# Performance work log

Hardware: AMD Instinct MI355X
Metric: run time of the kernel (lower is better)

The kernel has to match this reference:

```python
import jax, jax.numpy as jnp
import numpy as np

CLAMP_LO, CLAMP_HI, CLAMP_GATE_MAX = -10.0, 10.0, 10.0
E, TOPK = 8, 2
M, K, N = 2048, 2048, 1408  # tokens, hidden_dim, intermediate_dim
CAPACITY = 2 * (M * TOPK // E)


def setup_inputs() -> dict:
    key = jax.random.key(0)
    ks = jax.random.split(key, 6)
    bk = 1.0 / np.sqrt(K)  # kaiming_uniform(a=sqrt(5)) bound = 1/sqrt(fan_in)
    bn = 1.0 / np.sqrt(N)
    return {
        "flat_h": jax.random.normal(ks[0], (M, K), jnp.float32),
        "flat_idx": jax.random.randint(ks[1], (M, TOPK), 0, E),
        "flat_gate": jax.random.uniform(ks[2], (M, TOPK), jnp.float32),
        "gate_weight": jax.random.uniform(ks[3], (E, N, K), jnp.float32, -bk, bk),
        "up_weight": jax.random.uniform(ks[4], (E, N, K), jnp.float32, -bk, bk),
        "down_weight": jax.random.uniform(ks[5], (E, K, N), jnp.float32, -bn, bn),
    }


def reference(flat_h, flat_idx, flat_gate, gate_weight, up_weight, down_weight):
    m, top_k = flat_idx.shape
    k = flat_h.shape[1]
    e = gate_weight.shape[0]
    r = m * top_k

    expert_id = flat_idx.reshape(-1)                                   # (R,)
    gate = flat_gate.reshape(-1)                                       # (R,)
    token_index = jnp.repeat(jnp.arange(m, dtype=jnp.int32), top_k)    # (R,)

    # stable sort rows by expert id (mirrors torch.argsort(..., stable=True))
    sort_idx = jnp.argsort(expert_id, stable=True)
    sorted_eid = expert_id[sort_idx]
    tok_sorted = token_index[sort_idx]
    gate_sorted = gate[sort_idx]

    # position of each sorted row inside its expert group
    counts = jnp.bincount(expert_id, length=e)
    starts = jnp.concatenate([jnp.zeros(1, counts.dtype), jnp.cumsum(counts)[:-1]])
    pos = jnp.arange(r) - starts[sorted_eid]                           # (R,)

    # dispatch: scatter sorted tokens into fixed-capacity (E, C, K) buffer
    buf = jnp.zeros((e, CAPACITY, k), flat_h.dtype)
    buf = buf.at[sorted_eid, pos].set(flat_h[tok_sorted])

    # grouped GEMMs: weights stored (E, out, in) like nn.Linear
    g = jnp.einsum("eck,enk->ecn", buf, gate_weight)
    g = jnp.minimum(g, CLAMP_GATE_MAX)
    u = jnp.clip(jnp.einsum("eck,enk->ecn", buf, up_weight), CLAMP_LO, CLAMP_HI)
    h = jax.nn.silu(g) * u                                             # SwiGLU (E, C, N)
    d = jnp.einsum("ecn,ekn->eck", h, down_weight)                     # (E, C, K)

    # combine: gather each routed row back, weight by gate, sum over top_k slots
    expert_out = d[sorted_eid, pos]                                    # (R, K)
    weighted = expert_out * gate_sorted[:, None]
    out = jnp.zeros((m, k), flat_h.dtype).at[tok_sorted].add(weighted)
    return out
```

## Files before the change

### kernel.cpp

```cpp
#include <hip/hip_runtime.h>
#include <hip/hip_bf16.h>

#define M_TOK 2048
#define KDIM 2048
#define NDIM 1408
#define NEXP 8
#define RROWS (M_TOK * 2)
#define CAP 1024

typedef __attribute__((ext_vector_type(8))) short short8;
typedef __attribute__((ext_vector_type(4))) float f32x4;

__device__ __forceinline__ unsigned short bf16rn(float f) {
    unsigned int u = __builtin_bit_cast(unsigned int, f);
    u += 0x7FFFu + ((u >> 16) & 1u);
    return (unsigned short)(u >> 16);
}
__device__ __forceinline__ unsigned int pk2(float a, float b) {
    return (unsigned int)bf16rn(a) | ((unsigned int)bf16rn(b) << 16);
}
__device__ __forceinline__ unsigned int cvtpk(float a, float b) {
    __hip_bfloat162 h = __float22bfloat162_rn(make_float2(a, b));
    unsigned int u;
    __builtin_memcpy(&u, &h, 4);
    return u;
}

__device__ __forceinline__ void glds16(const void* g, void* l) {
    __builtin_amdgcn_global_load_lds(
        (const __attribute__((address_space(1))) unsigned int*)g,
        (__attribute__((address_space(3))) unsigned int*)l, 16, 0, 0);
}

__global__ void k_route(const float* __restrict__ h, const int* __restrict__ idx,
                        int* __restrict__ cnt, int* __restrict__ slot_of,
                        unsigned short* __restrict__ bufA) {
    int r = blockIdx.x;
    __shared__ int s_ep;
    if (threadIdx.x == 0) {
        int e = idx[r];
        int p = atomicAdd(&cnt[e], 1);
        int ep = e * CAP + p;
        slot_of[r] = ep;
        s_ep = ep;
    }
    __syncthreads();
    int ep = s_ep;
    const float4* src = (const float4*)(h + (size_t)(r >> 1) * KDIM) + threadIdx.x * 2;
    float4 a = src[0], b = src[1];
    uint4 o;
    o.x = pk2(a.x, a.y); o.y = pk2(a.z, a.w);
    o.z = pk2(b.x, b.y); o.w = pk2(b.z, b.w);
    *((uint4*)(bufA + (size_t)ep * KDIM) + threadIdx.x) = o;
}

__global__ __launch_bounds__(256)
void k_reorder(const float* __restrict__ in, unsigned short* __restrict__ out,
               int R, int C) {
    const int e = blockIdx.x;
    const int slab = blockIdx.y;
    const int span = blockIdx.z;
    const int NC = C >> 6;
    const int tid = threadIdx.x;
    const int wave = tid >> 6, lane = tid & 63;
    const int c = span * 256 + lane * 4;
    if (c >= C) return;
    const int r0 = slab * 64 + wave * 16;
    const float* src = in + ((size_t)e * R + r0) * C + c;
    unsigned short* dst = out + (((size_t)e * NC + (c >> 6)) * R + r0) * 64 + (c & 63);
#pragma unroll
    for (int i = 0; i < 16; i++) {
        float4 v = *(const float4*)(src + (size_t)i * C);
        uint2 o;
        o.x = cvtpk(v.x, v.y);
        o.y = cvtpk(v.z, v.w);
        *(uint2*)(dst + i * 64) = o;
    }
}

__global__ __launch_bounds__(256, 2)
void k_gemm1(const unsigned short* __restrict__ bufA,
             const unsigned short* __restrict__ gwb,
             const unsigned short* __restrict__ uwb,
             const int* __restrict__ cnt, unsigned short* __restrict__ hbuf) {
    const int f = blockIdx.x;
    const int e = f & 7;
    const int t = f >> 3;
    const int n_blk = t % 22;
    const int m_blk = t / 22;
    const int m0 = m_blk * 128;
    if (m0 >= cnt[e]) return;
    const int n0 = n_blk * 64;

    const unsigned short* A = bufA + (size_t)e * CAP * KDIM;
    const unsigned short* Gc = gwb + (size_t)e * 32 * NDIM * 64;
    const unsigned short* Uc = uwb + (size_t)e * 32 * NDIM * 64;

    __shared__ unsigned short sA[2][128 * 64];
    __shared__ unsigned short sG[2][64 * 64];
    __shared__ unsigned short sU[2][64 * 64];

    const int tid = threadIdx.x;
    const int lane = tid & 63;
    const int wave = tid >> 6;
    const int wm = (wave >> 1) * 64, wn = (wave & 1) * 32;
    const int q = lane >> 4, l15 = lane & 15;
    const int sr = lane >> 3;
    const int scb = (lane & 7) ^ (sr & 7);
    const int xi = l15 & 7;
    const int cbl0 = (q ^ xi) * 8;
    const int cbl1 = ((4 + q) ^ xi) * 8;

    f32x4 accG[4][2] = {};
    f32x4 accU[4][2] = {};

#define STAGE1(kc, b) do {                                                              \
        _Pragma("unroll")                                                               \
        for (int c_ = 0; c_ < 4; c_++) {                                                \
            int seg = wave * 4 + c_;                                                    \
            glds16(A + (size_t)(m0 + seg * 8 + sr) * KDIM + (kc) * 64 + scb * 8,        \
                   &sA[b][seg * 512]);                                                  \
        }                                                                               \
        _Pragma("unroll")                                                               \
        for (int c_ = 0; c_ < 2; c_++) {                                                \
            int seg = wave * 2 + c_;                                                    \
            glds16(Gc + ((size_t)(kc) * NDIM + n0 + seg * 8 + sr) * 64 + scb * 8,       \
                   &sG[b][seg * 512]);                                                  \
            glds16(Uc + ((size_t)(kc) * NDIM + n0 + seg * 8 + sr) * 64 + scb * 8,       \
                   &sU[b][seg * 512]);                                                  \
        }                                                                               \
    } while (0)

    STAGE1(0, 0);

    for (int kc = 0; kc < 32; kc++) {
        const int cur = kc & 1;
        asm volatile("s_waitcnt vmcnt(0)" ::: "memory");
        __builtin_amdgcn_sched_barrier(0);
        __builtin_amdgcn_s_barrier();
        __builtin_amdgcn_sched_barrier(0);
        if (kc + 1 < 32) STAGE1(kc + 1, cur ^ 1);

#pragma unroll
        for (int kh = 0; kh < 2; kh++) {
            const int co = kh ? cbl1 : cbl0;
            short8 af[4], gf[2], uf[2];
#pragma unroll
            for (int i = 0; i < 4; i++)
                af[i] = *(const short8*)&sA[cur][(wm + i * 16 + l15) * 64 + co];
#pragma unroll
            for (int j = 0; j < 2; j++) {
                gf[j] = *(const short8*)&sG[cur][(wn + j * 16 + l15) * 64 + co];
                uf[j] = *(const short8*)&sU[cur][(wn + j * 16 + l15) * 64 + co];
            }
#pragma unroll
            for (int i = 0; i < 4; i++)
#pragma unroll
                for (int j = 0; j < 2; j++) {
                    accG[i][j] = __builtin_amdgcn_mfma_f32_16x16x32_bf16(af[i], gf[j], accG[i][j], 0, 0, 0);
                    accU[i][j] = __builtin_amdgcn_mfma_f32_16x16x32_bf16(af[i], uf[j], accU[i][j], 0, 0, 0);
                }
        }
    }
#undef STAGE1

    unsigned short* H = hbuf + (size_t)e * CAP * NDIM;
#pragma unroll
    for (int i = 0; i < 4; i++)
#pragma unroll
        for (int j = 0; j < 2; j++) {
            int col = n0 + wn + j * 16 + l15;
#pragma unroll
            for (int rg = 0; rg < 4; rg++) {
                int row = m0 + wm + i * 16 + q * 4 + rg;
                float g = accG[i][j][rg];
                float u = accU[i][j][rg];
                g = fminf(g, 10.f);
                u = fminf(fmaxf(u, -10.f), 10.f);
                float hv = g / (1.f + __expf(-g)) * u;
                H[(size_t)row * NDIM + col] = bf16rn(hv);
            }
        }
}

__global__ __launch_bounds__(256, 3)
void k_gemm2(const unsigned short* __restrict__ hbuf,
             const unsigned short* __restrict__ dwb, const int* __restrict__ cnt,
             float* __restrict__ dbuf) {
    const int f = blockIdx.x;
    const int e = f & 7;
    const int t = f >> 3;
    const int n_blk = t & 31;
    const int m_blk = t >> 5;
    const int cnt_e = cnt[e];
    const int m0 = m_blk * 128;
    if (m0 >= cnt_e) return;
    const int n0 = n_blk * 64;

    const unsigned short* Ah = hbuf + (size_t)e * CAP * NDIM;
    const unsigned short* Dc = dwb + (size_t)e * 22 * KDIM * 64;

    __shared__ unsigned short sA[2][128 * 64];
    __shared__ unsigned short sB[2][64 * 64];

    const int tid = threadIdx.x;
    const int lane = tid & 63;
    const int wave = tid >> 6;
    const int wm = (wave >> 1) * 64, wn = (wave & 1) * 32;
    const int q = lane >> 4, l15 = lane & 15;
    const int sr = lane >> 3;
    const int scb = (lane & 7) ^ (sr & 7);
    const int xi = l15 & 7;
    const int cbl0 = (q ^ xi) * 8;
    const int cbl1 = ((4 + q) ^ xi) * 8;

    f32x4 acc[4][2] = {};

#define STAGE2(nc, b) do {                                                              \
        _Pragma("unroll")                                                               \
        for (int c_ = 0; c_ < 4; c_++) {                                                \
            int seg = wave * 4 + c_;                                                    \
            glds16(Ah + (size_t)(m0 + seg * 8 + sr) * NDIM + (nc) * 64 + scb * 8,       \
                   &sA[b][seg * 512]);                                                  \
        }                                                                               \
        _Pragma("unroll")                                                               \
        for (int c_ = 0; c_ < 2; c_++) {                                                \
            int seg = wave * 2 + c_;                                                    \
            glds16(Dc + ((size_t)(nc) * KDIM + n0 + seg * 8 + sr) * 64 + scb * 8,       \
                   &sB[b][seg * 512]);                                                  \
        }                                                                               \
    } while (0)

    STAGE2(0, 0);

    for (int nc = 0; nc < 22; nc++) {
        const int cur = nc & 1;
        asm volatile("s_waitcnt vmcnt(0)" ::: "memory");
        __builtin_amdgcn_sched_barrier(0);
        __builtin_amdgcn_s_barrier();
        __builtin_amdgcn_sched_barrier(0);
        if (nc + 1 < 22) STAGE2(nc + 1, cur ^ 1);

#pragma unroll
        for (int kh = 0; kh < 2; kh++) {
            const int co = kh ? cbl1 : cbl0;
            short8 af[4], bfr[2];
#pragma unroll
            for (int i = 0; i < 4; i++)
                af[i] = *(const short8*)&sA[cur][(wm + i * 16 + l15) * 64 + co];
#pragma unroll
            for (int j = 0; j < 2; j++)
                bfr[j] = *(const short8*)&sB[cur][(wn + j * 16 + l15) * 64 + co];
#pragma unroll
            for (int i = 0; i < 4; i++)
#pragma unroll
                for (int j = 0; j < 2; j++)
                    acc[i][j] = __builtin_amdgcn_mfma_f32_16x16x32_bf16(af[i], bfr[j], acc[i][j], 0, 0, 0);
        }
    }
#undef STAGE2

    float* D = dbuf + (size_t)e * CAP * KDIM;
#pragma unroll
    for (int i = 0; i < 4; i++) {
#pragma unroll
        for (int rg = 0; rg < 4; rg++) {
            int row = m0 + wm + i * 16 + q * 4 + rg;
            if (row < cnt_e) {
                float* drow = D + (size_t)row * KDIM + n0 + wn + l15;
#pragma unroll
                for (int j = 0; j < 2; j++)
                    drow[j * 16] = acc[i][j][rg];
            }
        }
    }
}

__global__ void k_combine(const float* __restrict__ dbuf, const int* __restrict__ slot_of,
                          const float* __restrict__ gate, float* __restrict__ out) {
    int tk = blockIdx.x;
    int s0 = slot_of[2 * tk], s1 = slot_of[2 * tk + 1];
    float g0 = gate[2 * tk], g1 = gate[2 * tk + 1];
    const float4* r0 = (const float4*)(dbuf + (size_t)s0 * KDIM);
    const float4* r1 = (const float4*)(dbuf + (size_t)s1 * KDIM);
    float4* o = (float4*)(out + (size_t)tk * KDIM);
    int i = threadIdx.x * 2;
#pragma unroll
    for (int c = 0; c < 2; c++) {
        float4 a = r0[i + c], b = r1[i + c];
        float4 v;
        v.x = g0 * a.x + g1 * b.x;
        v.y = g0 * a.y + g1 * b.y;
        v.z = g0 * a.z + g1 * b.z;
        v.w = g0 * a.w + g1 * b.w;
        o[i + c] = v;
    }
}

extern "C" void kernel_launch(void* const* d_in, const int* in_sizes, int n_in,
                              void* d_out, int out_size, void* d_ws, size_t ws_size,
                              hipStream_t stream) {
    const float* flat_h = (const float*)d_in[0];
    const int* flat_idx = (const int*)d_in[1];
    const float* flat_gate = (const float*)d_in[2];
    const float* gw = (const float*)d_in[3];
    const float* uw = (const float*)d_in[4];
    const float* dwn = (const float*)d_in[5];
    float* out = (float*)d_out;

    char* w = (char*)d_ws;
    int* cnt = (int*)w;
    int* slot_of = (int*)(w + 256);
    unsigned short* bufA = (unsigned short*)(w + 1048576ull);
    unsigned short* hbuf = (unsigned short*)(w + 34603008ull);
    unsigned short* gwb  = (unsigned short*)(w + 57671680ull);
    unsigned short* uwb  = (unsigned short*)(w + 103809024ull);
    unsigned short* dwb  = (unsigned short*)(w + 149946368ull);
    float* dbuf = (float*)(w + 57671680ull);

    hipMemsetAsync(cnt, 0, 256, stream);

    k_route<<<RROWS, 256, 0, stream>>>(flat_h, flat_idx, cnt, slot_of, bufA);
    k_reorder<<<dim3(8, 22, 8), 256, 0, stream>>>(gw, gwb, NDIM, KDIM);
    k_reorder<<<dim3(8, 22, 8), 256, 0, stream>>>(uw, uwb, NDIM, KDIM);
    k_reorder<<<dim3(8, 32, 6), 256, 0, stream>>>(dwn, dwb, KDIM, NDIM);
    k_gemm1<<<8 * 22 * 8, 256, 0, stream>>>(bufA, gwb, uwb, cnt, hbuf);
    k_gemm2<<<8 * 32 * 8, 256, 0, stream>>>(hbuf, dwb, cnt, dbuf);
    k_combine<<<M_TOK, 256, 0, stream>>>(dbuf, slot_of, flat_gate, out);
}
```

Baseline: 514.6 us.

## Triple-buffer weight tiles in both GEMMs and fuse weight reorder launches

Both grouped GEMMs now keep three LDS buffers for the weight tiles and prefetch them two K-steps ahead, while activations stay double-buffered. Partial `s_waitcnt vmcnt` values replace the full drain, so only the current step's loads must land before the barrier. The three weight conversion and reorder launches are merged into one kernel that moves 8 floats per lane instead of 4. The cost is more LDS per block: k_gemm2's launch bounds drop from 3 to 2 blocks per CU, which may reduce latency hiding there.

```diff
diff --git a/kernel.cpp b/kernel.cpp
--- a/kernel.cpp
+++ b/kernel.cpp
@@ -55,26 +55,39 @@
 }
 
 __global__ __launch_bounds__(256)
-void k_reorder(const float* __restrict__ in, unsigned short* __restrict__ out,
-               int R, int C) {
-    const int e = blockIdx.x;
-    const int slab = blockIdx.y;
-    const int span = blockIdx.z;
-    const int NC = C >> 6;
+void k_reorder3(const float* __restrict__ gw, const float* __restrict__ uw,
+                const float* __restrict__ dwn,
+                unsigned short* __restrict__ gwb, unsigned short* __restrict__ uwb,
+                unsigned short* __restrict__ dwb) {
+    const int y = blockIdx.y;
+    const int t = blockIdx.x;
+    int R, C, spans;
+    const float* in;
+    unsigned short* out;
+    if (y == 2) { R = KDIM; C = NDIM; spans = 3; in = dwn; out = dwb; }
+    else { R = NDIM; C = KDIM; spans = 4; in = (y ? uw : gw); out = (y ? uwb : gwb); }
+    const int per_e = (R >> 6) * spans;
+    if (t >= NEXP * per_e) return;
+    const int e = t / per_e;
+    const int rem = t % per_e;
+    const int slab = rem / spans;
+    const int span = rem % spans;
     const int tid = threadIdx.x;
     const int wave = tid >> 6, lane = tid & 63;
-    const int c = span * 256 + lane * 4;
+    const int c = span * 512 + lane * 8;
     if (c >= C) return;
     const int r0 = slab * 64 + wave * 16;
+    const int NC = C >> 6;
     const float* src = in + ((size_t)e * R + r0) * C + c;
     unsigned short* dst = out + (((size_t)e * NC + (c >> 6)) * R + r0) * 64 + (c & 63);
 #pragma unroll
     for (int i = 0; i < 16; i++) {
-        float4 v = *(const float4*)(src + (size_t)i * C);
-        uint2 o;
-        o.x = cvtpk(v.x, v.y);
-        o.y = cvtpk(v.z, v.w);
-        *(uint2*)(dst + i * 64) = o;
+        float4 v0 = *(const float4*)(src + (size_t)i * C);
+        float4 v1 = *(const float4*)(src + (size_t)i * C + 4);
+        uint4 o;
+        o.x = cvtpk(v0.x, v0.y); o.y = cvtpk(v0.z, v0.w);
+        o.z = cvtpk(v1.x, v1.y); o.w = cvtpk(v1.z, v1.w);
+        *(uint4*)(dst + i * 64) = o;
     }
 }
 
@@ -97,8 +110,8 @@
     const unsigned short* Uc = uwb + (size_t)e * 32 * NDIM * 64;
 
     __shared__ unsigned short sA[2][128 * 64];
-    __shared__ unsigned short sG[2][64 * 64];
-    __shared__ unsigned short sU[2][64 * 64];
+    __shared__ unsigned short sG[3][64 * 64];
+    __shared__ unsigned short sU[3][64 * 64];
 
     const int tid = threadIdx.x;
     const int lane = tid & 63;
@@ -114,13 +127,15 @@
     f32x4 accG[4][2] = {};
     f32x4 accU[4][2] = {};
 
-#define STAGE1(kc, b) do {                                                              \
+#define STAGE_A1(kc, b) do {                                                            \
         _Pragma("unroll")                                                               \
         for (int c_ = 0; c_ < 4; c_++) {                                                \
             int seg = wave * 4 + c_;                                                    \
             glds16(A + (size_t)(m0 + seg * 8 + sr) * KDIM + (kc) * 64 + scb * 8,        \
                    &sA[b][seg * 512]);                                                  \
         }                                                                               \
+    } while (0)
+#define STAGE_W1(kc, b) do {                                                            \
         _Pragma("unroll")                                                               \
         for (int c_ = 0; c_ < 2; c_++) {                                                \
             int seg = wave * 2 + c_;                                                    \
@@ -131,15 +146,23 @@
         }                                                                               \
     } while (0)
 
-    STAGE1(0, 0);
+    STAGE_A1(0, 0);
+    STAGE_W1(0, 0);
+    STAGE_W1(1, 1);
 
     for (int kc = 0; kc < 32; kc++) {
         const int cur = kc & 1;
-        asm volatile("s_waitcnt vmcnt(0)" ::: "memory");
+        const int wcur = kc % 3;
+        if (kc == 31) {
+            asm volatile("s_waitcnt vmcnt(0)" ::: "memory");
+        } else {
+            asm volatile("s_waitcnt vmcnt(4)" ::: "memory");
+        }
         __builtin_amdgcn_sched_barrier(0);
         __builtin_amdgcn_s_barrier();
         __builtin_amdgcn_sched_barrier(0);
-        if (kc + 1 < 32) STAGE1(kc + 1, cur ^ 1);
+        if (kc + 1 < 32) STAGE_A1(kc + 1, cur ^ 1);
+        if (kc + 2 < 32) STAGE_W1(kc + 2, (kc + 2) % 3);
 
 #pragma unroll
         for (int kh = 0; kh < 2; kh++) {
@@ -150,8 +173,8 @@
                 af[i] = *(const short8*)&sA[cur][(wm + i * 16 + l15) * 64 + co];
 #pragma unroll
             for (int j = 0; j < 2; j++) {
-                gf[j] = *(const short8*)&sG[cur][(wn + j * 16 + l15) * 64 + co];
-                uf[j] = *(const short8*)&sU[cur][(wn + j * 16 + l15) * 64 + co];
+                gf[j] = *(const short8*)&sG[wcur][(wn + j * 16 + l15) * 64 + co];
+                uf[j] = *(const short8*)&sU[wcur][(wn + j * 16 + l15) * 64 + co];
             }
 #pragma unroll
             for (int i = 0; i < 4; i++)
@@ -162,7 +185,8 @@
                 }
         }
     }
-#undef STAGE1
+#undef STAGE_A1
+#undef STAGE_W1
 
     unsigned short* H = hbuf + (size_t)e * CAP * NDIM;
 #pragma unroll
@@ -183,7 +207,7 @@
         }
 }
 
-__global__ __launch_bounds__(256, 3)
+__global__ __launch_bounds__(256, 2)
 void k_gemm2(const unsigned short* __restrict__ hbuf,
              const unsigned short* __restrict__ dwb, const int* __restrict__ cnt,
              float* __restrict__ dbuf) {
@@ -201,7 +225,7 @@
     const unsigned short* Dc = dwb + (size_t)e * 22 * KDIM * 64;
 
     __shared__ unsigned short sA[2][128 * 64];
-    __shared__ unsigned short sB[2][64 * 64];
+    __shared__ unsigned short sB[3][64 * 64];
 
     const int tid = threadIdx.x;
     const int lane = tid & 63;
@@ -216,13 +240,15 @@
 
     f32x4 acc[4][2] = {};
 
-#define STAGE2(nc, b) do {                                                              \
+#define STAGE_A2(nc, b) do {                                                            \
         _Pragma("unroll")                                                               \
         for (int c_ = 0; c_ < 4; c_++) {                                                \
             int seg = wave * 4 + c_;                                                    \
             glds16(Ah + (size_t)(m0 + seg * 8 + sr) * NDIM + (nc) * 64 + scb * 8,       \
                    &sA[b][seg * 512]);                                                  \
         }                                                                               \
+    } while (0)
+#define STAGE_W2(nc, b) do {                                                            \
         _Pragma("unroll")                                                               \
         for (int c_ = 0; c_ < 2; c_++) {                                                \
             int seg = wave * 2 + c_;                                                    \
@@ -231,15 +257,23 @@
         }                                                                               \
     } while (0)
 
-    STAGE2(0, 0);
+    STAGE_A2(0, 0);
+    STAGE_W2(0, 0);
+    STAGE_W2(1, 1);
 
     for (int nc = 0; nc < 22; nc++) {
         const int cur = nc & 1;
-        asm volatile("s_waitcnt vmcnt(0)" ::: "memory");
+        const int wcur = nc % 3;
+        if (nc == 21) {
+            asm volatile("s_waitcnt vmcnt(0)" ::: "memory");
+        } else {
+            asm volatile("s_waitcnt vmcnt(2)" ::: "memory");
+        }
         __builtin_amdgcn_sched_barrier(0);
         __builtin_amdgcn_s_barrier();
         __builtin_amdgcn_sched_barrier(0);
-        if (nc + 1 < 22) STAGE2(nc + 1, cur ^ 1);
+        if (nc + 1 < 22) STAGE_A2(nc + 1, cur ^ 1);
+        if (nc + 2 < 22) STAGE_W2(nc + 2, (nc + 2) % 3);
 
 #pragma unroll
         for (int kh = 0; kh < 2; kh++) {
@@ -250,7 +284,7 @@
                 af[i] = *(const short8*)&sA[cur][(wm + i * 16 + l15) * 64 + co];
 #pragma unroll
             for (int j = 0; j < 2; j++)
-                bfr[j] = *(const short8*)&sB[cur][(wn + j * 16 + l15) * 64 + co];
+                bfr[j] = *(const short8*)&sB[wcur][(wn + j * 16 + l15) * 64 + co];
 #pragma unroll
             for (int i = 0; i < 4; i++)
 #pragma unroll
@@ -258,7 +292,8 @@
                     acc[i][j] = __builtin_amdgcn_mfma_f32_16x16x32_bf16(af[i], bfr[j], acc[i][j], 0, 0, 0);
         }
     }
-#undef STAGE2
+#undef STAGE_A2
+#undef STAGE_W2
 
     float* D = dbuf + (size_t)e * CAP * KDIM;
 #pragma unroll
@@ -321,9 +356,7 @@
     hipMemsetAsync(cnt, 0, 256, stream);
 
     k_route<<<RROWS, 256, 0, stream>>>(flat_h, flat_idx, cnt, slot_of, bufA);
-    k_reorder<<<dim3(8, 22, 8), 256, 0, stream>>>(gw, gwb, NDIM, KDIM);
-    k_reorder<<<dim3(8, 22, 8), 256, 0, stream>>>(uw, uwb, NDIM, KDIM);
-    k_reorder<<<dim3(8, 32, 6), 256, 0, stream>>>(dwn, dwb, KDIM, NDIM);
+    k_reorder3<<<dim3(768, 3), 256, 0, stream>>>(gw, uw, dwn, gwb, uwb, dwb);
     k_gemm1<<<8 * 22 * 8, 256, 0, stream>>>(bufA, gwb, uwb, cnt, hbuf);
     k_gemm2<<<8 * 32 * 8, 256, 0, stream>>>(hbuf, dwb, cnt, dbuf);
     k_combine<<<M_TOK, 256, 0, stream>>>(dbuf, slot_of, flat_gate, out);
```

Measured after the change: 533.2 us. 3.6% more time.

## Fuse fp32-to-bf16 weight conversion into GEMM register loads, drop reorder kernels

Applied to the files above, without the earlier changes.

Removes the three weight reorder/convert kernels and has each GEMM load fp32 weights straight from global memory into registers, converting them to bf16 MFMA fragments in the loop with a one-step register prefetch. This avoids writing and re-reading a bf16 copy of all weights. In exchange, every M-block re-reads fp32 weights (twice the bytes of bf16), with per-lane 32-byte strided row loads that coalesce worse, and pays conversion ALU work plus extra register pressure in the GEMM loop.

```diff
diff --git a/kernel.cpp b/kernel.cpp
--- a/kernel.cpp
+++ b/kernel.cpp
@@ -24,6 +24,14 @@
     unsigned int u;
     __builtin_memcpy(&u, &h, 4);
     return u;
+}
+__device__ __forceinline__ short8 mk8(float4 a, float4 b) {
+    uint4 o;
+    o.x = cvtpk(a.x, a.y); o.y = cvtpk(a.z, a.w);
+    o.z = cvtpk(b.x, b.y); o.w = cvtpk(b.z, b.w);
+    short8 r;
+    __builtin_memcpy(&r, &o, 16);
+    return r;
 }
 
 __device__ __forceinline__ void glds16(const void* g, void* l) {
@@ -54,34 +62,10 @@
     *((uint4*)(bufA + (size_t)ep * KDIM) + threadIdx.x) = o;
 }
 
-__global__ __launch_bounds__(256)
-void k_reorder(const float* __restrict__ in, unsigned short* __restrict__ out,
-               int R, int C) {
-    const int e = blockIdx.x;
-    const int slab = blockIdx.y;
-    const int span = blockIdx.z;
-    const int NC = C >> 6;
-    const int tid = threadIdx.x;
-    const int wave = tid >> 6, lane = tid & 63;
-    const int c = span * 256 + lane * 4;
-    if (c >= C) return;
-    const int r0 = slab * 64 + wave * 16;
-    const float* src = in + ((size_t)e * R + r0) * C + c;
-    unsigned short* dst = out + (((size_t)e * NC + (c >> 6)) * R + r0) * 64 + (c & 63);
-#pragma unroll
-    for (int i = 0; i < 16; i++) {
-        float4 v = *(const float4*)(src + (size_t)i * C);
-        uint2 o;
-        o.x = cvtpk(v.x, v.y);
-        o.y = cvtpk(v.z, v.w);
-        *(uint2*)(dst + i * 64) = o;
-    }
-}
-
 __global__ __launch_bounds__(256, 2)
 void k_gemm1(const unsigned short* __restrict__ bufA,
-             const unsigned short* __restrict__ gwb,
-             const unsigned short* __restrict__ uwb,
+             const float* __restrict__ gw,
+             const float* __restrict__ uw,
              const int* __restrict__ cnt, unsigned short* __restrict__ hbuf) {
     const int f = blockIdx.x;
     const int e = f & 7;
@@ -93,12 +77,10 @@
     const int n0 = n_blk * 64;
 
     const unsigned short* A = bufA + (size_t)e * CAP * KDIM;
-    const unsigned short* Gc = gwb + (size_t)e * 32 * NDIM * 64;
-    const unsigned short* Uc = uwb + (size_t)e * 32 * NDIM * 64;
+    const float* G = gw + (size_t)e * NDIM * KDIM;
+    const float* U = uw + (size_t)e * NDIM * KDIM;
 
     __shared__ unsigned short sA[2][128 * 64];
-    __shared__ unsigned short sG[2][64 * 64];
-    __shared__ unsigned short sU[2][64 * 64];
 
     const int tid = threadIdx.x;
     const int lane = tid & 63;
@@ -111,27 +93,38 @@
     const int cbl0 = (q ^ xi) * 8;
     const int cbl1 = ((4 + q) ^ xi) * 8;
 
+    const float* Gr = G + (size_t)(n0 + wn + l15) * KDIM + q * 8;
+    const float* Ur = U + (size_t)(n0 + wn + l15) * KDIM + q * 8;
+
     f32x4 accG[4][2] = {};
     f32x4 accU[4][2] = {};
 
-#define STAGE1(kc, b) do {                                                              \
+    float4 sg[2][2][2], su[2][2][2];
+
+#define STAGE_A1(kc, b) do {                                                            \
         _Pragma("unroll")                                                               \
         for (int c_ = 0; c_ < 4; c_++) {                                                \
             int seg = wave * 4 + c_;                                                    \
             glds16(A + (size_t)(m0 + seg * 8 + sr) * KDIM + (kc) * 64 + scb * 8,        \
                    &sA[b][seg * 512]);                                                  \
         }                                                                               \
-        _Pragma("unroll")                                                               \
-        for (int c_ = 0; c_ < 2; c_++) {                                                \
-            int seg = wave * 2 + c_;                                                    \
-            glds16(Gc + ((size_t)(kc) * NDIM + n0 + seg * 8 + sr) * 64 + scb * 8,       \
-                   &sG[b][seg * 512]);                                                  \
-            glds16(Uc + ((size_t)(kc) * NDIM + n0 + seg * 8 + sr) * 64 + scb * 8,       \
-                   &sU[b][seg * 512]);                                                  \
+    } while (0)
+#define LOAD_W1(kc) do {                                                                \
+        _Pragma("unroll")                                                               \
+        for (int j_ = 0; j_ < 2; j_++)                                                  \
+        _Pragma("unroll")                                                               \
+        for (int kh_ = 0; kh_ < 2; kh_++) {                                             \
+            const float* gp = Gr + (size_t)j_ * 16 * KDIM + (kc) * 64 + kh_ * 32;       \
+            sg[j_][kh_][0] = *(const float4*)gp;                                        \
+            sg[j_][kh_][1] = *(const float4*)(gp + 4);                                  \
+            const float* up = Ur + (size_t)j_ * 16 * KDIM + (kc) * 64 + kh_ * 32;       \
+            su[j_][kh_][0] = *(const float4*)up;                                        \
+            su[j_][kh_][1] = *(const float4*)(up + 4);                                  \
         }                                                                               \
     } while (0)
 
-    STAGE1(0, 0);
+    STAGE_A1(0, 0);
+    LOAD_W1(0);
 
     for (int kc = 0; kc < 32; kc++) {
         const int cur = kc & 1;
@@ -139,30 +132,39 @@
         __builtin_amdgcn_sched_barrier(0);
         __builtin_amdgcn_s_barrier();
         __builtin_amdgcn_sched_barrier(0);
-        if (kc + 1 < 32) STAGE1(kc + 1, cur ^ 1);
+
+        short8 gf[2][2], uf[2][2];
+#pragma unroll
+        for (int j = 0; j < 2; j++)
+#pragma unroll
+            for (int kh = 0; kh < 2; kh++) {
+                gf[kh][j] = mk8(sg[j][kh][0], sg[j][kh][1]);
+                uf[kh][j] = mk8(su[j][kh][0], su[j][kh][1]);
+            }
+
+        if (kc + 1 < 32) {
+            STAGE_A1(kc + 1, cur ^ 1);
+            LOAD_W1(kc + 1);
+        }
 
 #pragma unroll
         for (int kh = 0; kh < 2; kh++) {
             const int co = kh ? cbl1 : cbl0;
-            short8 af[4], gf[2], uf[2];
+            short8 af[4];
 #pragma unroll
             for (int i = 0; i < 4; i++)
                 af[i] = *(const short8*)&sA[cur][(wm + i * 16 + l15) * 64 + co];
 #pragma unroll
-            for (int j = 0; j < 2; j++) {
-                gf[j] = *(const short8*)&sG[cur][(wn + j * 16 + l15) * 64 + co];
-                uf[j] = *(const short8*)&sU[cur][(wn + j * 16 + l15) * 64 + co];
-            }
-#pragma unroll
             for (int i = 0; i < 4; i++)
 #pragma unroll
                 for (int j = 0; j < 2; j++) {
-                    accG[i][j] = __builtin_amdgcn_mfma_f32_16x16x32_bf16(af[i], gf[j], accG[i][j], 0, 0, 0);
-                    accU[i][j] = __builtin_amdgcn_mfma_f32_16x16x32_bf16(af[i], uf[j], accU[i][j], 0, 0, 0);
+                    accG[i][j] = __builtin_amdgcn_mfma_f32_16x16x32_bf16(af[i], gf[kh][j], accG[i][j], 0, 0, 0);
+                    accU[i][j] = __builtin_amdgcn_mfma_f32_16x16x32_bf16(af[i], uf[kh][j], accU[i][j], 0, 0, 0);
                 }
         }
     }
-#undef STAGE1
+#undef STAGE_A1
+#undef LOAD_W1
 
     unsigned short* H = hbuf + (size_t)e * CAP * NDIM;
 #pragma unroll
@@ -185,7 +187,7 @@
 
 __global__ __launch_bounds__(256, 3)
 void k_gemm2(const unsigned short* __restrict__ hbuf,
-             const unsigned short* __restrict__ dwb, const int* __restrict__ cnt,
+             const float* __restrict__ dwn, const int* __restrict__ cnt,
              float* __restrict__ dbuf) {
     const int f = blockIdx.x;
     const int e = f & 7;
@@ -198,10 +200,9 @@
     const int n0 = n_blk * 64;
 
     const unsigned short* Ah = hbuf + (size_t)e * CAP * NDIM;
-    const unsigned short* Dc = dwb + (size_t)e * 22 * KDIM * 64;
+    const float* B = dwn + (size_t)e * KDIM * NDIM;
 
     __shared__ unsigned short sA[2][128 * 64];
-    __shared__ unsigned short sB[2][64 * 64];
 
     const int tid = threadIdx.x;
     const int lane = tid & 63;
@@ -214,24 +215,32 @@
     const int cbl0 = (q ^ xi) * 8;
     const int cbl1 = ((4 + q) ^ xi) * 8;
 
+    const float* Br = B + (size_t)(n0 + wn + l15) * NDIM + q * 8;
+
     f32x4 acc[4][2] = {};
-
-#define STAGE2(nc, b) do {                                                              \
+    float4 sb[2][2][2];
+
+#define STAGE_A2(nc, b) do {                                                            \
         _Pragma("unroll")                                                               \
         for (int c_ = 0; c_ < 4; c_++) {                                                \
             int seg = wave * 4 + c_;                                                    \
             glds16(Ah + (size_t)(m0 + seg * 8 + sr) * NDIM + (nc) * 64 + scb * 8,       \
                    &sA[b][seg * 512]);                                                  \
         }                                                                               \
-        _Pragma("unroll")                                                               \
-        for (int c_ = 0; c_ < 2; c_++) {                                                \
-            int seg = wave * 2 + c_;                                                    \
-            glds16(Dc + ((size_t)(nc) * KDIM + n0 + seg * 8 + sr) * 64 + scb * 8,       \
-                   &sB[b][seg * 512]);                                                  \
+    } while (0)
+#define LOAD_W2(nc) do {                                                                \
+        _Pragma("unroll")                                                               \
+        for (int j_ = 0; j_ < 2; j_++)                                                  \
+        _Pragma("unroll")                                                               \
+        for (int kh_ = 0; kh_ < 2; kh_++) {                                             \
+            const float* bp = Br + (size_t)j_ * 16 * NDIM + (nc) * 64 + kh_ * 32;       \
+            sb[j_][kh_][0] = *(const float4*)bp;                                        \
+            sb[j_][kh_][1] = *(const float4*)(bp + 4);                                  \
         }                                                                               \
     } while (0)
 
-    STAGE2(0, 0);
+    STAGE_A2(0, 0);
+    LOAD_W2(0);
 
     for (int nc = 0; nc < 22; nc++) {
         const int cur = nc & 1;
@@ -239,26 +248,35 @@
         __builtin_amdgcn_sched_barrier(0);
         __builtin_amdgcn_s_barrier();
         __builtin_amdgcn_sched_barrier(0);
-        if (nc + 1 < 22) STAGE2(nc + 1, cur ^ 1);
+
+        short8 bf2[2][2];
+#pragma unroll
+        for (int j = 0; j < 2; j++)
+#pragma unroll
+            for (int kh = 0; kh < 2; kh++)
+                bf2[kh][j] = mk8(sb[j][kh][0], sb[j][kh][1]);
+
+        if (nc + 1 < 22) {
+            STAGE_A2(nc + 1, cur ^ 1);
+            LOAD_W2(nc + 1);
+        }
 
 #pragma unroll
         for (int kh = 0; kh < 2; kh++) {
             const int co = kh ? cbl1 : cbl0;
-            short8 af[4], bfr[2];
+            short8 af[4];
 #pragma unroll
             for (int i = 0; i < 4; i++)
                 af[i] = *(const short8*)&sA[cur][(wm + i * 16 + l15) * 64 + co];
 #pragma unroll
-            for (int j = 0; j < 2; j++)
-                bfr[j] = *(const short8*)&sB[cur][(wn + j * 16 + l15) * 64 + co];
-#pragma unroll
             for (int i = 0; i < 4; i++)
 #pragma unroll
                 for (int j = 0; j < 2; j++)
-                    acc[i][j] = __builtin_amdgcn_mfma_f32_16x16x32_bf16(af[i], bfr[j], acc[i][j], 0, 0, 0);
-        }
-    }
-#undef STAGE2
+                    acc[i][j] = __builtin_amdgcn_mfma_f32_16x16x32_bf16(af[i], bf2[kh][j], acc[i][j], 0, 0, 0);
+        }
+    }
+#undef STAGE_A2
+#undef LOAD_W2
 
     float* D = dbuf + (size_t)e * CAP * KDIM;
 #pragma unroll
@@ -313,18 +331,12 @@
     int* slot_of = (int*)(w + 256);
     unsigned short* bufA = (unsigned short*)(w + 1048576ull);
     unsigned short* hbuf = (unsigned short*)(w + 34603008ull);
-    unsigned short* gwb  = (unsigned short*)(w + 57671680ull);
-    unsigned short* uwb  = (unsigned short*)(w + 103809024ull);
-    unsigned short* dwb  = (unsigned short*)(w + 149946368ull);
     float* dbuf = (float*)(w + 57671680ull);
 
     hipMemsetAsync(cnt, 0, 256, stream);
 
     k_route<<<RROWS, 256, 0, stream>>>(flat_h, flat_idx, cnt, slot_of, bufA);
-    k_reorder<<<dim3(8, 22, 8), 256, 0, stream>>>(gw, gwb, NDIM, KDIM);
-    k_reorder<<<dim3(8, 22, 8), 256, 0, stream>>>(uw, uwb, NDIM, KDIM);
-    k_reorder<<<dim3(8, 32, 6), 256, 0, stream>>>(dwn, dwb, KDIM, NDIM);
-    k_gemm1<<<8 * 22 * 8, 256, 0, stream>>>(bufA, gwb, uwb, cnt, hbuf);
-    k_gemm2<<<8 * 32 * 8, 256, 0, stream>>>(hbuf, dwb, cnt, dbuf);
+    k_gemm1<<<8 * 22 * 8, 256, 0, stream>>>(bufA, gw, uw, cnt, hbuf);
+    k_gemm2<<<8 * 32 * 8, 256, 0, stream>>>(hbuf, dwn, cnt, dbuf);
     k_combine<<<M_TOK, 256, 0, stream>>>(dbuf, slot_of, flat_gate, out);
 }
```

Result: slower. 657.4 us (+27.8%).
